# Performance work log

Measured on AMD Instinct MI355X. Metric: run time of the kernel, lower is better.

The kernel has to match this reference:

```python
import jax, jax.numpy as jnp
import numpy as np

HOP = 128
NFFT = 256
SR = 16000
EPS = 1e-7
MIN_DB = -80.0


def _a_weighting_db():
    # librosa.fft_frequencies + librosa.A_weighting (min_db=-80), computed statically in numpy
    f = np.fft.rfftfreq(NFFT, d=1.0 / SR)  # [NFFT//2+1]
    c = np.array([12194.217, 20.598997, 107.65265, 737.86223]) ** 2.0
    f2 = f ** 2.0
    w = 2.0 + 20.0 * (
        np.log10(c[0])
        + 2.0 * np.log10(np.maximum(f2, 1e-30))
        - np.log10(f2 + c[0])
        - np.log10(f2 + c[1])
        - 0.5 * np.log10(f2 + c[2])
        - 0.5 * np.log10(f2 + c[3])
    )
    return np.maximum(w, MIN_DB).astype(np.float32)


def _loudness(x):
    # x: [B, C, T] -> channel mean -> librosa-style centered STFT (hann, reflect pad)
    x = jnp.mean(x, axis=1)  # [B, T]
    T = x.shape[1]
    pad = NFFT // 2
    xp = jnp.pad(x, ((0, 0), (pad, pad)), mode='reflect')  # [B, T+NFFT]
    n_frames = 1 + T // HOP
    idx = jnp.arange(n_frames)[:, None] * HOP + jnp.arange(NFFT)[None, :]  # [F, NFFT]
    frames = xp[:, idx]  # [B, F, NFFT]
    # periodic hann window (scipy fftbins=True, librosa default)
    win = (0.5 - 0.5 * jnp.cos(2.0 * jnp.pi * jnp.arange(NFFT) / NFFT)).astype(x.dtype)
    spec = jnp.fft.rfft(frames * win, axis=-1)  # [B, F, NFFT//2+1] complex
    log_mag = jnp.log(jnp.abs(spec) + EPS)  # [B, F, NFREQ]
    aw = jnp.asarray(_a_weighting_db())  # [NFREQ]
    # mean over frequency axis, then trailing singleton like original unsqueeze(-1)
    loud = jnp.mean(log_mag + aw[None, None, :], axis=-1)  # [B, F]
    return loud[..., None].astype(jnp.float32)


def setup_inputs() -> dict:
    key = jax.random.key(0)
    x = jax.random.normal(key, (64, 1, 640000), dtype=jnp.float32)
    return {"x": x}


def reference(x):
    return _loudness(x)
```

## Files before the change

### kernel.cpp

```cpp
#include <hip/hip_runtime.h>
#include <math.h>

#define HOP 128
#define T_LEN 640000
#define N_FRAMES 5001
#define N_PAIRS 2501
#define NB 64
#define GPB 16

#define RE_SLOT 18
#define RE_GRP  164
#define IM_SLOT 18
#define IM_GRP  132

typedef float v2f __attribute__((ext_vector_type(2)));

static __device__ __forceinline__ v2f mk2(float a, float b) { v2f r; r.x = a; r.y = b; return r; }
static __device__ __forceinline__ v2f sp(float s) { v2f r; r.x = s; r.y = s; return r; }

static __device__ __forceinline__ float rsum16(float v) {
    v += __int_as_float(__builtin_amdgcn_update_dpp(0, __float_as_int(v), 0xB1, 0xF, 0xF, true));
    v += __int_as_float(__builtin_amdgcn_update_dpp(0, __float_as_int(v), 0x4E, 0xF, 0xF, true));
    v += __int_as_float(__builtin_amdgcn_update_dpp(0, __float_as_int(v), 0x141, 0xF, 0xF, true));
    v += __int_as_float(__builtin_amdgcn_update_dpp(0, __float_as_int(v), 0x140, 0xF, 0xF, true));
    return v;
}

__global__ __launch_bounds__(256) void setup_kernel(float* __restrict__ ws) {
    __shared__ float s_aw[132];
    const int tid = threadIdx.x;
    const float TP = 0.02454369260617026f;
    {
        const int w = tid >> 4, rr = tid & 15;
        float s, c;
        sincosf((float)(rr * w) * TP, &s, &c);
        ((v2f*)ws)[tid] = mk2(c, -s);
    }
    if (tid < 129) {
        const float LG2_10 = 0.30102999566398f;
        float fq = (float)tid * 62.5f;
        float f2 = fq * fq;
        const float a0 = 12194.217f * 12194.217f;
        const float a1 = 20.598997f * 20.598997f;
        const float a2 = 107.65265f * 107.65265f;
        const float a3 = 737.86223f * 737.86223f;
        float w = 2.0f + 20.0f * LG2_10 *
                  (__builtin_amdgcn_logf(a0) + 2.0f * __builtin_amdgcn_logf(fmaxf(f2, 1e-30f))
                 - __builtin_amdgcn_logf(f2 + a0) - __builtin_amdgcn_logf(f2 + a1)
                 - 0.5f * __builtin_amdgcn_logf(f2 + a2) - 0.5f * __builtin_amdgcn_logf(f2 + a3));
        s_aw[tid] = fmaxf(w, -80.0f);
    }
    __syncthreads();
    if (tid < 16) {
        float s = 0.f;
#pragma unroll
        for (int k2 = 0; k2 < 8; ++k2) s += s_aw[tid + 16 * k2];
        ws[512 + tid] = s;
        if (tid == 0) ws[528] = s_aw[128];
    }
}

__global__ __launch_bounds__(256) void loudness_kernel(const float* __restrict__ x,
                                                       float* __restrict__ out,
                                                       const float* __restrict__ ws) {
    constexpr float C16[16] = {
        1.0f,  0.9238795325112867f,  0.7071067811865476f,  0.3826834323650898f,
        0.0f, -0.3826834323650898f, -0.7071067811865476f, -0.9238795325112867f,
       -1.0f, -0.9238795325112867f, -0.7071067811865476f, -0.3826834323650898f,
        0.0f,  0.3826834323650898f,  0.7071067811865476f,  0.9238795325112867f};
    constexpr float S16[16] = {
        0.0f,  0.3826834323650898f,  0.7071067811865476f,  0.9238795325112867f,
        1.0f,  0.9238795325112867f,  0.7071067811865476f,  0.3826834323650898f,
        0.0f, -0.3826834323650898f, -0.7071067811865476f, -0.9238795325112867f,
       -1.0f, -0.9238795325112867f, -0.7071067811865476f, -0.3826834323650898f};
    const float R2  = 0.7071067811865476f;
    const float c1v = 0.9238795325112867f, s1v = 0.3826834323650898f;
    const float c3v = 0.3826834323650898f, s3v = 0.9238795325112867f;
    const float CP8 = 0.9238795325112867f, SP8 = 0.3826834323650898f;
    const float K2  = 1.8477590650225735f;

    __shared__ alignas(16) v2f s_re[16 * RE_GRP];
    __shared__ alignas(16) v2f s_im[16 * IM_GRP];
    __shared__ v2f s_twT[256];

    const int tid = threadIdx.x;
    const int g = tid >> 4;
    const int r = tid & 15;

    s_twT[tid] = ((const v2f*)ws)[tid];
    const float aw8r  = ws[512 + r];
    const float aw128 = ws[528];
    const v2f stp = ((const v2f*)ws)[16 + r];

    float win16[16];
    {
        float cm2 = stp.x;
        float cm1 = stp.x * CP8 + stp.y * SP8;
        win16[0] = 0.5f - 0.5f * cm2;
        win16[1] = 0.5f - 0.5f * cm1;
#pragma unroll
        for (int n = 2; n < 16; ++n) {
            const float c = K2 * cm1 - cm2;
            win16[n] = 0.5f - 0.5f * c;
            cm2 = cm1; cm1 = c;
        }
    }
    __syncthreads();

    const int gp = blockIdx.x * GPB + g;
    const int b  = gp / N_PAIRS;
    const int pp = gp - b * N_PAIRS;
    const int fA = 2 * pp;
    const int fB = (fA < 5000) ? fA + 1 : 5000;
    const int dB = (fB - fA) * HOP;
    const float* __restrict__ xb = x + (size_t)b * T_LEN;

    v2f xw[16];
    const int base = fA * HOP - HOP + r;
    if (pp >= 1 && pp <= 2499) {
        const float* __restrict__ xp = xb + base;
        float s24[24];
#pragma unroll
        for (int j = 0; j < 24; ++j) s24[j] = xp[16 * j];
#pragma unroll
        for (int n2 = 0; n2 < 16; ++n2)
            xw[n2] = mk2(s24[n2], s24[n2 + 8]) * sp(win16[n2]);
    } else {
#pragma unroll
        for (int n2 = 0; n2 < 16; ++n2) {
            int jA = base + 16 * n2;
            int jB = jA + dB;
            jA = (jA < 0) ? -jA : jA;
            jA = (jA >= T_LEN) ? (2 * T_LEN - 2 - jA) : jA;
            jB = (jB < 0) ? -jB : jB;
            jB = (jB >= T_LEN) ? (2 * T_LEN - 2 - jB) : jB;
            xw[n2] = mk2(xb[jA], xb[jB]) * sp(win16[n2]);
        }
    }

    v2f pv[8], qv[8];
#pragma unroll
    for (int n = 1; n <= 7; ++n) { pv[n] = xw[n] + xw[16 - n]; qv[n] = xw[n] - xw[16 - n]; }
    const v2f bse = xw[0] + xw[8];
    const v2f d08 = xw[0] - xw[8];
    const v2f se  = pv[2] + pv[4] + pv[6];
    const v2f so  = pv[1] + pv[3] + pv[5] + pv[7];
    const v2f r0  = bse + se + so;
    const v2f r8  = bse + se - so;
    v2f rre[8], rim[8];
#pragma unroll
    for (int k1 = 1; k1 <= 7; ++k1) {
        v2f re = (k1 & 1) ? d08 : bse;
        v2f im = sp(0.f);
#pragma unroll
        for (int n = 1; n <= 7; ++n) {
            const int m = (k1 * n) & 15;
            re += pv[n] * sp(C16[m]);
            im -= qv[n] * sp(S16[m]);
        }
        rre[k1] = re;
        rim[k1] = im;
    }

    {
        v2f* __restrict__ reW = &s_re[g * RE_GRP + r];
        v2f* __restrict__ imW = &s_im[g * IM_GRP + r];
        reW[0] = r0;
#pragma unroll
        for (int k = 1; k <= 7; ++k) {
            reW[RE_SLOT * k] = rre[k];
            imW[IM_SLOT * (k - 1)] = rim[k];
        }
        reW[RE_SLOT * 8] = r8;
    }

    const int rp  = (r <= 8) ? r : 16 - r;
    const int rpi = (rp >= 1 && rp <= 7) ? (rp - 1) : 0;
    const float ysgn = (r == 0 || r == 8) ? 0.f : ((r < 8) ? 1.f : -1.f);
    const float4* __restrict__ reCol = (const float4*)&s_re[g * RE_GRP + RE_SLOT * rp];
    const float4* __restrict__ imCol = (const float4*)&s_im[g * IM_GRP + IM_SLOT * rpi];
    const v2f* __restrict__ twp = &s_twT[r];

    v2f bbx[16], bby[16];
#pragma unroll
    for (int j = 0; j < 8; ++j) {
        const float4 R4v = reCol[j];
        const float4 I4v = imCol[j];
        {
            const int w = 2 * j;
            const v2f tw = twp[16 * w];
            const v2f xx = mk2(R4v.x, R4v.y);
            const v2f yy = mk2(I4v.x, I4v.y) * sp(ysgn);
            bbx[w] = xx * sp(tw.x) - yy * sp(tw.y);
            bby[w] = xx * sp(tw.y) + yy * sp(tw.x);
        }
        {
            const int w = 2 * j + 1;
            const v2f tw = twp[16 * w];
            const v2f xx = mk2(R4v.z, R4v.w);
            const v2f yy = mk2(I4v.z, I4v.w) * sp(ysgn);
            bbx[w] = xx * sp(tw.x) - yy * sp(tw.y);
            bby[w] = xx * sp(tw.y) + yy * sp(tw.x);
        }
    }

#pragma unroll
    for (int j = 0; j < 8; ++j) {
        const v2f ux = bbx[j], uy = bby[j], vx = bbx[j + 8], vy = bby[j + 8];
        bbx[j] = ux + vx; bby[j] = uy + vy;
        const v2f dx = ux - vx, dy = uy - vy;
        v2f ox, oy;
        if      (j == 0) { ox = dx;                              oy = dy; }
        else if (j == 1) { ox =  dx * sp(c1v) + dy * sp(s1v);    oy =  dy * sp(c1v) - dx * sp(s1v); }
        else if (j == 2) { ox = (dx + dy) * sp(R2);              oy = (dy - dx) * sp(R2); }
        else if (j == 3) { ox =  dx * sp(c3v) + dy * sp(s3v);    oy =  dy * sp(c3v) - dx * sp(s3v); }
        else if (j == 4) { ox = dy;                              oy = sp(0.f) - dx; }
        else if (j == 5) { ox = dy * sp(s3v) - dx * sp(c3v);     oy = sp(0.f) - dy * sp(c3v) - dx * sp(s3v); }
        else if (j == 6) { ox = (dy - dx) * sp(R2);              oy = sp(0.f) - (dx + dy) * sp(R2); }
        else             { ox = dy * sp(s1v) - dx * sp(c1v);     oy = sp(0.f) - dy * sp(c1v) - dx * sp(s1v); }
        bbx[j + 8] = ox; bby[j + 8] = oy;
    }
#pragma unroll
    for (int h = 0; h <= 8; h += 8) {
#pragma unroll
        for (int j = 0; j < 4; ++j) {
            const v2f ux = bbx[h + j], uy = bby[h + j], vx = bbx[h + j + 4], vy = bby[h + j + 4];
            bbx[h + j] = ux + vx; bby[h + j] = uy + vy;
            const v2f dx = ux - vx, dy = uy - vy;
            v2f ox, oy;
            if      (j == 0) { ox = dx;                  oy = dy; }
            else if (j == 1) { ox = (dx + dy) * sp(R2);  oy = (dy - dx) * sp(R2); }
            else if (j == 2) { ox = dy;                  oy = sp(0.f) - dx; }
            else             { ox = (dy - dx) * sp(R2);  oy = sp(0.f) - (dx + dy) * sp(R2); }
            bbx[h + j + 4] = ox; bby[h + j + 4] = oy;
        }
    }
#pragma unroll
    for (int gg = 0; gg < 16; gg += 4) {
        {
            const v2f ux = bbx[gg], uy = bby[gg], vx = bbx[gg + 2], vy = bby[gg + 2];
            bbx[gg] = ux + vx;     bby[gg] = uy + vy;
            bbx[gg + 2] = ux - vx; bby[gg + 2] = uy - vy;
        }
        {
            const v2f ux = bbx[gg + 1], uy = bby[gg + 1], vx = bbx[gg + 3], vy = bby[gg + 3];
            bbx[gg + 1] = ux + vx; bby[gg + 1] = uy + vy;
            const v2f dx = ux - vx, dy = uy - vy;
            bbx[gg + 3] = dy; bby[gg + 3] = sp(0.f) - dx;
        }
    }

    const float HALF_LN2 = 0.34657359027997264f;
    v2f m2[8];
#pragma unroll
    for (int t = 0; t < 8; ++t) {
        const v2f Yx = bbx[2 * t] + bbx[2 * t + 1];
        const v2f Yy = bby[2 * t] + bby[2 * t + 1];
        m2[t] = Yx * Yx + Yy * Yy + sp(1e-14f);
    }
    const v2f P0 = m2[0] * m2[1], P1 = m2[2] * m2[3], P2 = m2[4] * m2[5], P3 = m2[6] * m2[7];
    const float lA = __builtin_amdgcn_logf(P0.x) + __builtin_amdgcn_logf(P1.x)
                   + __builtin_amdgcn_logf(P2.x) + __builtin_amdgcn_logf(P3.x);
    const float lB = __builtin_amdgcn_logf(P0.y) + __builtin_amdgcn_logf(P1.y)
                   + __builtin_amdgcn_logf(P2.y) + __builtin_amdgcn_logf(P3.y);
    v2f ssum = sp(HALF_LN2) * mk2(lA, lB) + sp(aw8r);

    const v2f d0 = bbx[0] - bbx[1];
    if (r == 0) {
        ssum += sp(HALF_LN2) * mk2(__builtin_amdgcn_logf(d0.x * d0.x + 1e-14f),
                                   __builtin_amdgcn_logf(d0.y * d0.y + 1e-14f))
              + sp(aw128);
    }

    ssum.x = rsum16(ssum.x);
    ssum.y = rsum16(ssum.y);

    if (r == 0) {
        out[b * N_FRAMES + fA] = ssum.x * (1.0f / 129.0f);
        out[b * N_FRAMES + fB] = ssum.y * (1.0f / 129.0f);
    }
}

extern "C" void kernel_launch(void* const* d_in, const int* in_sizes, int n_in,
                              void* d_out, int out_size, void* d_ws, size_t ws_size,
                              hipStream_t stream) {
    const float* x = (const float*)d_in[0];
    float* out = (float*)d_out;
    float* ws = (float*)d_ws;
    setup_kernel<<<1, 256, 0, stream>>>(ws);
    loudness_kernel<<<(NB * N_PAIRS) / GPB, 256, 0, stream>>>(x, out, ws);
}
```

Baseline: 55.38 us.

## Apply FFT twiddles before LDS transpose and drop shared twiddle table

Moves the inter-stage twiddle multiply to the writer side, where each lane generates its twiddles by complex recurrence from a per-lane step instead of reading a 256-entry shared table. The reader side now uses compile-time cos/sin constants selected by a lo/hi flag to form conjugate-symmetric outputs. This removes the twiddle table load, its LDS storage and one block-wide barrier. In exchange the imaginary LDS buffer grows to hold an extra slot, and the recurrence may accumulate small rounding error.

After: 57.41 us. 3.7% more time.

```diff
diff --git a/kernel.cpp b/kernel.cpp
--- a/kernel.cpp
+++ b/kernel.cpp
@@ -11,7 +11,7 @@
 #define RE_SLOT 18
 #define RE_GRP  164
 #define IM_SLOT 18
-#define IM_GRP  132
+#define IM_GRP  146
 
 typedef float v2f __attribute__((ext_vector_type(2)));
 
@@ -81,13 +81,11 @@
 
     __shared__ alignas(16) v2f s_re[16 * RE_GRP];
     __shared__ alignas(16) v2f s_im[16 * IM_GRP];
-    __shared__ v2f s_twT[256];
 
     const int tid = threadIdx.x;
     const int g = tid >> 4;
     const int r = tid & 15;
 
-    s_twT[tid] = ((const v2f*)ws)[tid];
     const float aw8r  = ws[512 + r];
     const float aw128 = ws[528];
     const v2f stp = ((const v2f*)ws)[16 + r];
@@ -105,7 +103,6 @@
             cm2 = cm1; cm1 = c;
         }
     }
-    __syncthreads();
 
     const int gp = blockIdx.x * GPB + g;
     const int b  = gp / N_PAIRS;
@@ -166,20 +163,25 @@
         v2f* __restrict__ reW = &s_re[g * RE_GRP + r];
         v2f* __restrict__ imW = &s_im[g * IM_GRP + r];
         reW[0] = r0;
+        float twx = stp.x, twy = stp.y;
 #pragma unroll
         for (int k = 1; k <= 7; ++k) {
-            reW[RE_SLOT * k] = rre[k];
-            imW[IM_SLOT * (k - 1)] = rim[k];
-        }
-        reW[RE_SLOT * 8] = r8;
+            reW[RE_SLOT * k]       = rre[k] * sp(twx) - rim[k] * sp(twy);
+            imW[IM_SLOT * (k - 1)] = rre[k] * sp(twy) + rim[k] * sp(twx);
+            const float nx = twx * stp.x - twy * stp.y;
+            const float ny = twx * stp.y + twy * stp.x;
+            twx = nx; twy = ny;
+        }
+        reW[RE_SLOT * 8] = r8 * sp(twx);
+        imW[IM_SLOT * 7] = r8 * sp(twy);
     }
 
     const int rp  = (r <= 8) ? r : 16 - r;
-    const int rpi = (rp >= 1 && rp <= 7) ? (rp - 1) : 0;
-    const float ysgn = (r == 0 || r == 8) ? 0.f : ((r < 8) ? 1.f : -1.f);
+    const int rpi = (rp >= 1) ? (rp - 1) : 0;
+    const bool lo = (r <= 8);
+    const float y0 = (r == 0) ? 0.f : 1.f;
     const float4* __restrict__ reCol = (const float4*)&s_re[g * RE_GRP + RE_SLOT * rp];
     const float4* __restrict__ imCol = (const float4*)&s_im[g * IM_GRP + IM_SLOT * rpi];
-    const v2f* __restrict__ twp = &s_twT[r];
 
     v2f bbx[16], bby[16];
 #pragma unroll
@@ -188,19 +190,23 @@
         const float4 I4v = imCol[j];
         {
             const int w = 2 * j;
-            const v2f tw = twp[16 * w];
-            const v2f xx = mk2(R4v.x, R4v.y);
-            const v2f yy = mk2(I4v.x, I4v.y) * sp(ysgn);
-            bbx[w] = xx * sp(tw.x) - yy * sp(tw.y);
-            bby[w] = xx * sp(tw.y) + yy * sp(tw.x);
+            const float Aw = lo ? 1.f : C16[w];
+            const float Bw = lo ? 0.f : S16[w];
+            const float Ew = lo ? y0  : -C16[w];
+            const v2f Zx = mk2(R4v.x, R4v.y);
+            const v2f Zy = mk2(I4v.x, I4v.y);
+            bbx[w] = Zx * sp(Aw) - Zy * sp(Bw);
+            bby[w] = Zy * sp(Ew) - Zx * sp(Bw);
         }
         {
             const int w = 2 * j + 1;
-            const v2f tw = twp[16 * w];
-            const v2f xx = mk2(R4v.z, R4v.w);
-            const v2f yy = mk2(I4v.z, I4v.w) * sp(ysgn);
-            bbx[w] = xx * sp(tw.x) - yy * sp(tw.y);
-            bby[w] = xx * sp(tw.y) + yy * sp(tw.x);
+            const float Aw = lo ? 1.f : C16[w];
+            const float Bw = lo ? 0.f : S16[w];
+            const float Ew = lo ? y0  : -C16[w];
+            const v2f Zx = mk2(R4v.z, R4v.w);
+            const v2f Zy = mk2(I4v.z, I4v.w);
+            bbx[w] = Zx * sp(Aw) - Zy * sp(Bw);
+            bby[w] = Zy * sp(Ew) - Zx * sp(Bw);
         }
     }
 
```
